# Optimization experiments

Hardware: AMD Instinct MI355X
Metric: run time of the kernel (lower is better)

Reference implementation:

```python
import jax, jax.numpy as jnp
import numpy as np

ALPHA = 0.2  # LeakyReLU negative slope
NEG_INF = -9e15

def setup_inputs() -> dict:
    key = jax.random.key(0)
    k1, k2, k3, k4 = jax.random.split(key, 4)
    N, IN_F, OUT_F = 12288, 256, 128
    h = jax.random.normal(k1, (N, IN_F), dtype=jnp.float32)
    adj = jax.random.randint(k2, (N, N), 0, 2, dtype=jnp.int32)
    # Xavier-uniform-like init with gain 1.414
    limW = 1.414 * np.sqrt(6.0 / (IN_F + OUT_F))
    W = jax.random.uniform(k3, (IN_F, OUT_F), dtype=jnp.float32, minval=-limW, maxval=limW)
    lima = 1.414 * np.sqrt(6.0 / (2 * OUT_F + 1))
    a = jax.random.uniform(k4, (2 * OUT_F, 1), dtype=jnp.float32, minval=-lima, maxval=lima)
    return {"h": h, "adj": adj, "W": W, "a": a}

def reference(h, adj, W, a):
    out_f = W.shape[1]
    Wh = h @ W                      # [N, out_f]
    Wh1 = Wh @ a[:out_f, :]         # [N, 1]
    Wh2 = Wh @ a[out_f:, :]         # [N, 1]
    e = Wh1 + Wh2.T                 # [N, N] broadcast-add scores
    e = jnp.where(e > 0, e, ALPHA * e)  # LeakyReLU
    scores = jnp.where(adj > 0, e, NEG_INF)
    attention = jax.nn.softmax(scores, axis=1)  # dropout is identity at inference
    h_prime = attention @ Wh        # [N, out_f]
    return jax.nn.elu(h_prime)      # concat=True -> ELU
```

## Files before the change

### kernel.cpp

```cpp
#include <hip/hip_runtime.h>

#define NN   12288
#define FIN  256
#define FOUT 128
#define ALPHA 0.2f

typedef __attribute__((ext_vector_type(8))) _Float16 half8v;
typedef __attribute__((ext_vector_type(4))) float float4v;
typedef __attribute__((ext_vector_type(4))) int   int4v;


#define GLL16(gp, lp)                                                          \
    __builtin_amdgcn_global_load_lds(                                          \
        (const __attribute__((address_space(1))) void*)(gp),                   \
        (__attribute__((address_space(3))) void*)(lp), 16, 0, 0)

__global__ __launch_bounds__(128) void k_wh(
    const float* __restrict__ h,
    const float* __restrict__ W,
    const float* __restrict__ a,
    _Float16* __restrict__ WhT2,
    float* __restrict__ Wh1, float* __restrict__ Wh2)
{
    __shared__ __align__(16) float hs[16 * FIN];
    __shared__ float sP1[2][16], sP2[2][16];
    const int t = threadIdx.x;
    const int row0 = blockIdx.x * 16;

    const float4v* hsrc = (const float4v*)(h + (size_t)row0 * FIN);
    float4v* hdst = (float4v*)hs;
    #pragma unroll
    for (int i = 0; i < 8; ++i) hdst[t + i * 128] = hsrc[t + i * 128];
    __syncthreads();

    float acc[16];
    #pragma unroll
    for (int r = 0; r < 16; ++r) acc[r] = 0.f;

    for (int k = 0; k < FIN; k += 4) {
        const float w0 = W[(k + 0) * FOUT + t];
        const float w1 = W[(k + 1) * FOUT + t];
        const float w2 = W[(k + 2) * FOUT + t];
        const float w3 = W[(k + 3) * FOUT + t];
        #pragma unroll
        for (int r = 0; r < 16; ++r) {
            const float4v hv = *(const float4v*)&hs[r * FIN + k];
            float s = acc[r];
            s = fmaf(hv.x, w0, s);
            s = fmaf(hv.y, w1, s);
            s = fmaf(hv.z, w2, s);
            s = fmaf(hv.w, w3, s);
            acc[r] = s;
        }
    }

    half8v pk0, pk1;
    #pragma unroll
    for (int r = 0; r < 8; ++r)  pk0[r] = (_Float16)acc[r];
    #pragma unroll
    for (int r = 0; r < 8; ++r)  pk1[r] = (_Float16)acc[8 + r];
    _Float16* dst = WhT2 + (size_t)(row0 >> 5) * 4096 + t * 32 + (row0 & 16);
    *(half8v*)(dst)     = pk0;
    *(half8v*)(dst + 8) = pk1;

    const float a1t = a[t];
    const float a2t = a[FOUT + t];
    const int lane = t & 63, wv = t >> 6;
    #pragma unroll
    for (int r = 0; r < 16; ++r) {
        float v1 = acc[r] * a1t;
        float v2 = acc[r] * a2t;
        #pragma unroll
        for (int off = 1; off < 64; off <<= 1) {
            v1 += __shfl_xor(v1, off, 64);
            v2 += __shfl_xor(v2, off, 64);
        }
        if (lane == 0) { sP1[wv][r] = v1; sP2[wv][r] = v2; }
    }
    __syncthreads();
    if (t < 16) {
        Wh1[row0 + t] = sP1[0][t] + sP1[1][t];
        Wh2[row0 + t] = sP2[0][t] + sP2[1][t];
    }
}

__global__ __launch_bounds__(256) void k_max(
    const float* __restrict__ Wh2, float* __restrict__ outmax)
{
    __shared__ float sm[4];
    float m = -1e30f;
    for (int i = threadIdx.x; i < NN; i += 256) m = fmaxf(m, Wh2[i]);
    #pragma unroll
    for (int off = 1; off < 64; off <<= 1) m = fmaxf(m, __shfl_xor(m, off, 64));
    if ((threadIdx.x & 63) == 0) sm[threadIdx.x >> 6] = m;
    __syncthreads();
    if (threadIdx.x == 0)
        outmax[0] = fmaxf(fmaxf(sm[0], sm[1]), fmaxf(sm[2], sm[3]));
}

static __device__ __forceinline__ half8v build_p(
    const int4v a0, const int4v a1, const float* wvv,
    const float wh1, const float M, float& S)
{
    const int av[8] = {a0.x, a0.y, a0.z, a0.w, a1.x, a1.y, a1.z, a1.w};
    half8v af;
    #pragma unroll
    for (int jj = 0; jj < 8; ++jj) {
        float e = wh1 + wvv[jj];
        e = fmaxf(e, ALPHA * e);
        const float p = av[jj] ? __expf(e - M) : 0.f;
        af[jj] = (_Float16)p;
        S += p;
    }
    return af;
}

__global__ __launch_bounds__(256, 3) void k_attn(
    const int* __restrict__ adj,
    const _Float16* __restrict__ WhT2,
    const float* __restrict__ Wh1, const float* __restrict__ Wh2,
    const float* __restrict__ maxp,
    float* __restrict__ pC, float* __restrict__ pS)
{
    __shared__ __align__(16) _Float16 tile[2][2][4096];
    const int tid  = threadIdx.x;
    const int w    = tid >> 6;
    const int lane = tid & 63;
    const int m    = lane & 15;
    const int q    = lane >> 4;
    const int rowbase = blockIdx.x * 128 + w * 32;
    const int J    = gridDim.y;
    const int jy   = blockIdx.y;
    const int jlen = NN / J;
    const int jbeg = jy * jlen;
    const int iters = jlen / 64;

    const float mxv  = maxp[0];
    const float wh1a = Wh1[rowbase + m];
    const float wh1b = Wh1[rowbase + 16 + m];
    const float tma = wh1a + mxv; const float Ma = fmaxf(tma, ALPHA * tma);
    const float tmb = wh1b + mxv; const float Mb = fmaxf(tmb, ALPHA * tmb);

    const int* rowA = adj + (size_t)(rowbase + m) * NN;
    const int* rowB = adj + (size_t)(rowbase + 16 + m) * NN;

    float4v c[2][8];
    #pragma unroll
    for (int rg = 0; rg < 2; ++rg)
        #pragma unroll
        for (int t = 0; t < 8; ++t) c[rg][t] = (float4v){0.f, 0.f, 0.f, 0.f};
    float Sa = 0.f, Sb = 0.f;

    {
        const float4v* grp = (const float4v*)(WhT2 + (size_t)(jbeg >> 5) * 4096);
        float4v* lb = (float4v*)&tile[0][0][0];
        #pragma unroll
        for (int k = 0; k < 4; ++k)
            GLL16(grp + (w * 4 + k) * 64 + lane, lb + (w * 4 + k) * 64);
    }
    __syncthreads();

    int buf = 0;
    for (int it = 0; it < iters; ++it) {
        const int j0 = jbeg + it * 64;

        if (it + 1 < iters) {
            const float4v* grp =
                (const float4v*)(WhT2 + (size_t)((j0 + 64) >> 5) * 4096);
            float4v* lb = (float4v*)&tile[buf ^ 1][0][0];
            #pragma unroll
            for (int k = 0; k < 4; ++k)
                GLL16(grp + (w * 4 + k) * 64 + lane, lb + (w * 4 + k) * 64);
        }

        const int jb0 = j0 + q * 8;
        const int jb1 = j0 + 32 + q * 8;
        const int4v aA0 = __builtin_nontemporal_load((const int4v*)(rowA + jb0));
        const int4v aA1 = __builtin_nontemporal_load((const int4v*)(rowA + jb0 + 4));
        const int4v aA2 = __builtin_nontemporal_load((const int4v*)(rowA + jb1));
        const int4v aA3 = __builtin_nontemporal_load((const int4v*)(rowA + jb1 + 4));
        const int4v aB0 = __builtin_nontemporal_load((const int4v*)(rowB + jb0));
        const int4v aB1 = __builtin_nontemporal_load((const int4v*)(rowB + jb0 + 4));
        const int4v aB2 = __builtin_nontemporal_load((const int4v*)(rowB + jb1));
        const int4v aB3 = __builtin_nontemporal_load((const int4v*)(rowB + jb1 + 4));
        const float4v w00 = *(const float4v*)(Wh2 + jb0);
        const float4v w01 = *(const float4v*)(Wh2 + jb0 + 4);
        const float4v w10 = *(const float4v*)(Wh2 + jb1);
        const float4v w11 = *(const float4v*)(Wh2 + jb1 + 4);
        const float wv0[8] = {w00.x, w00.y, w00.z, w00.w, w01.x, w01.y, w01.z, w01.w};
        const float wv1[8] = {w10.x, w10.y, w10.z, w10.w, w11.x, w11.y, w11.z, w11.w};

        const half8v afa0 = build_p(aA0, aA1, wv0, wh1a, Ma, Sa);
        const half8v afa1 = build_p(aA2, aA3, wv1, wh1a, Ma, Sa);
        const half8v afb0 = build_p(aB0, aB1, wv0, wh1b, Mb, Sb);
        const half8v afb1 = build_p(aB2, aB3, wv1, wh1b, Mb, Sb);

        #pragma unroll
        for (int t = 0; t < 8; ++t) {
            const half8v b = *(const half8v*)&tile[buf][0][(t * 16 + m) * 32 + q * 8];
            c[0][t] = __builtin_amdgcn_mfma_f32_16x16x32_f16(afa0, b, c[0][t], 0, 0, 0);
            c[1][t] = __builtin_amdgcn_mfma_f32_16x16x32_f16(afb0, b, c[1][t], 0, 0, 0);
        }
        #pragma unroll
        for (int t = 0; t < 8; ++t) {
            const half8v b = *(const half8v*)&tile[buf][1][(t * 16 + m) * 32 + q * 8];
            c[0][t] = __builtin_amdgcn_mfma_f32_16x16x32_f16(afa1, b, c[0][t], 0, 0, 0);
            c[1][t] = __builtin_amdgcn_mfma_f32_16x16x32_f16(afb1, b, c[1][t], 0, 0, 0);
        }

        __syncthreads();
        buf ^= 1;
    }

    Sa += __shfl_xor(Sa, 16, 64); Sa += __shfl_xor(Sa, 32, 64);
    Sb += __shfl_xor(Sb, 16, 64); Sb += __shfl_xor(Sb, 32, 64);
    if (q == 0) {
        pS[(size_t)jy * NN + rowbase + m]      = Sa;
        pS[(size_t)jy * NN + rowbase + 16 + m] = Sb;
    }
    #pragma unroll
    for (int rg = 0; rg < 2; ++rg)
        #pragma unroll
        for (int t = 0; t < 8; ++t)
            #pragma unroll
            for (int reg = 0; reg < 4; ++reg) {
                const int row = rowbase + rg * 16 + q * 4 + reg;
                pC[((size_t)jy * NN + row) * FOUT + t * 16 + m] = c[rg][t][reg];
            }
}

__global__ __launch_bounds__(256) void k_reduce(
    const float* __restrict__ pC, const float* __restrict__ pS,
    float* __restrict__ out, int J)
{
    const int idx = blockIdx.x * 256 + threadIdx.x;
    const int row = idx >> 5;
    const int c4  = (idx & 31) * 4;
    float4v acc = (float4v){0.f, 0.f, 0.f, 0.f};
    float S = 0.f;
    for (int j = 0; j < J; ++j) {
        const float4v v = *(const float4v*)(pC + ((size_t)j * NN + row) * FOUT + c4);
        acc.x += v.x; acc.y += v.y; acc.z += v.z; acc.w += v.w;
        S += pS[(size_t)j * NN + row];
    }
    const float inv = 1.f / fmaxf(S, 1e-30f);
    float4v r;
    #pragma unroll
    for (int k = 0; k < 4; ++k) {
        const float v = acc[k] * inv;
        r[k] = (v > 0.f) ? v : (__expf(v) - 1.f);
    }
    *(float4v*)(out + (size_t)row * FOUT + c4) = r;
}

__global__ __launch_bounds__(256) void k_attn_fb(
    const int* __restrict__ adj,
    const _Float16* __restrict__ WhT2,
    const float* __restrict__ Wh1, const float* __restrict__ Wh2,
    const float* __restrict__ maxp,
    float* __restrict__ out)
{
    __shared__ __align__(16) float cbuf[4][8][64][4];
    __shared__ float sbuf[4][16];
    const int tid  = threadIdx.x;
    const int w    = tid >> 6;
    const int lane = tid & 63;
    const int m    = lane & 15;
    const int q    = lane >> 4;
    const int i    = blockIdx.x * 16 + m;

    const float wh1 = Wh1[i];
    const float tm = wh1 + maxp[0];
    const float Mi = fmaxf(tm, ALPHA * tm);

    float4v c[8];
    #pragma unroll
    for (int t = 0; t < 8; ++t) c[t] = (float4v){0.f, 0.f, 0.f, 0.f};
    float S = 0.f;
    const int* adjrow = adj + (size_t)i * NN;

    for (int j0 = w * (NN / 4); j0 < (w + 1) * (NN / 4); j0 += 32) {
        const int jb = j0 + q * 8;
        const int4v  a0 = *(const int4v*)(adjrow + jb);
        const int4v  a1 = *(const int4v*)(adjrow + jb + 4);
        const float4v w0 = *(const float4v*)(Wh2 + jb);
        const float4v w1 = *(const float4v*)(Wh2 + jb + 4);
        half8v bfr[8];
        #pragma unroll
        for (int t = 0; t < 8; ++t)
            bfr[t] = *(const half8v*)(WhT2 + (size_t)(j0 >> 5) * 4096 + (t * 16 + m) * 32 + q * 8);
        const float wvv[8] = {w0.x, w0.y, w0.z, w0.w, w1.x, w1.y, w1.z, w1.w};
        const half8v af = build_p(a0, a1, wvv, wh1, Mi, S);
        #pragma unroll
        for (int t = 0; t < 8; ++t)
            c[t] = __builtin_amdgcn_mfma_f32_16x16x32_f16(af, bfr[t], c[t], 0, 0, 0);
    }
    S += __shfl_xor(S, 16, 64);
    S += __shfl_xor(S, 32, 64);
    if (lane < 16) sbuf[w][lane] = S;
    #pragma unroll
    for (int t = 0; t < 8; ++t) *(float4v*)&cbuf[w][t][lane][0] = c[t];
    __syncthreads();
    #pragma unroll
    for (int tt = 0; tt < 2; ++tt) {
        const int t = w * 2 + tt;
        float4v cs = *(const float4v*)&cbuf[0][t][lane][0];
        #pragma unroll
        for (int w2 = 1; w2 < 4; ++w2) {
            const float4v o = *(const float4v*)&cbuf[w2][t][lane][0];
            cs.x += o.x; cs.y += o.y; cs.z += o.z; cs.w += o.w;
        }
        #pragma unroll
        for (int reg = 0; reg < 4; ++reg) {
            const int mloc = q * 4 + reg;
            const float Sr = sbuf[0][mloc] + sbuf[1][mloc] + sbuf[2][mloc] + sbuf[3][mloc];
            const float v = cs[reg] / fmaxf(Sr, 1e-30f);
            out[(size_t)(blockIdx.x * 16 + mloc) * FOUT + t * 16 + m] =
                (v > 0.f) ? v : (__expf(v) - 1.f);
        }
    }
}

extern "C" void kernel_launch(void* const* d_in, const int* in_sizes, int n_in,
                              void* d_out, int out_size, void* d_ws, size_t ws_size,
                              hipStream_t stream) {
    const float* h   = (const float*)d_in[0];
    const int*   adj = (const int*)d_in[1];
    const float* W   = (const float*)d_in[2];
    const float* a   = (const float*)d_in[3];
    float* out = (float*)d_out;

    char* ws = (char*)d_ws;
    float* Wh1 = (float*)ws;
    float* Wh2 = (float*)(ws + 49152);
    float* mx  = (float*)(ws + 98304);
    _Float16* WhT2 = (_Float16*)(ws + 98560);
    const size_t base_need = 98560ULL + 3145728ULL;

    int J = 8;
    while (J > 1 &&
           base_need + (size_t)J * NN * 4 + (size_t)J * NN * FOUT * 4 > ws_size)
        J >>= 1;
    const bool ok =
        base_need + (size_t)NN * 4 + (size_t)NN * FOUT * 4 <= ws_size;

    k_wh  <<<NN / 16, 128, 0, stream>>>(h, W, a, WhT2, Wh1, Wh2);
    k_max <<<1, 256, 0, stream>>>(Wh2, mx);
    if (ok) {
        float* pS = (float*)(ws + base_need);
        float* pC = pS + (size_t)J * NN;
        k_attn<<<dim3(NN / 128, J), 256, 0, stream>>>(adj, WhT2, Wh1, Wh2, mx, pC, pS);
        k_reduce<<<(NN * (FOUT / 4)) / 256, 256, 0, stream>>>(pC, pS, out, J);
    } else {
        k_attn_fb<<<NN / 16, 256, 0, stream>>>(adj, WhT2, Wh1, Wh2, mx, out);
    }
}
```

Before: 880.9 us.

## Drop LDS staging, fuse max into projection, shrink attention tiles

The projection kernel now reads h straight from global memory instead of staging it in LDS. Each block also writes a per-block max of Wh2, so the separate max kernel is gone and every attention block reduces those partials itself. The attention kernel drops the double-buffered LDS tile of WhT2 and instead reads B fragments directly from global memory. Each wave now handles 16 rows instead of 32, so B fragments are reused across half as many rows and global/L2 traffic for WhT2 roughly doubles. The fallback kernel is reshaped the same way.

```diff
diff --git a/kernel.cpp b/kernel.cpp
--- a/kernel.cpp
+++ b/kernel.cpp
@@ -9,34 +9,24 @@
 typedef __attribute__((ext_vector_type(4))) float float4v;
 typedef __attribute__((ext_vector_type(4))) int   int4v;
 
-
-#define GLL16(gp, lp)                                                          \
-    __builtin_amdgcn_global_load_lds(                                          \
-        (const __attribute__((address_space(1))) void*)(gp),                   \
-        (__attribute__((address_space(3))) void*)(lp), 16, 0, 0)
 
 __global__ __launch_bounds__(128) void k_wh(
     const float* __restrict__ h,
     const float* __restrict__ W,
     const float* __restrict__ a,
     _Float16* __restrict__ WhT2,
-    float* __restrict__ Wh1, float* __restrict__ Wh2)
-{
-    __shared__ __align__(16) float hs[16 * FIN];
+    float* __restrict__ Wh1, float* __restrict__ Wh2,
+    float* __restrict__ mxArr)
+{
     __shared__ float sP1[2][16], sP2[2][16];
     const int t = threadIdx.x;
     const int row0 = blockIdx.x * 16;
 
-    const float4v* hsrc = (const float4v*)(h + (size_t)row0 * FIN);
-    float4v* hdst = (float4v*)hs;
-    #pragma unroll
-    for (int i = 0; i < 8; ++i) hdst[t + i * 128] = hsrc[t + i * 128];
-    __syncthreads();
-
     float acc[16];
     #pragma unroll
     for (int r = 0; r < 16; ++r) acc[r] = 0.f;
 
+    const float* hb = h + (size_t)row0 * FIN;
     for (int k = 0; k < FIN; k += 4) {
         const float w0 = W[(k + 0) * FOUT + t];
         const float w1 = W[(k + 1) * FOUT + t];
@@ -44,7 +34,7 @@
         const float w3 = W[(k + 3) * FOUT + t];
         #pragma unroll
         for (int r = 0; r < 16; ++r) {
-            const float4v hv = *(const float4v*)&hs[r * FIN + k];
+            const float4v hv = *(const float4v*)(hb + r * FIN + k);
             float s = acc[r];
             s = fmaf(hv.x, w0, s);
             s = fmaf(hv.y, w1, s);
@@ -79,23 +69,15 @@
     }
     __syncthreads();
     if (t < 16) {
-        Wh1[row0 + t] = sP1[0][t] + sP1[1][t];
-        Wh2[row0 + t] = sP2[0][t] + sP2[1][t];
-    }
-}
-
-__global__ __launch_bounds__(256) void k_max(
-    const float* __restrict__ Wh2, float* __restrict__ outmax)
-{
-    __shared__ float sm[4];
-    float m = -1e30f;
-    for (int i = threadIdx.x; i < NN; i += 256) m = fmaxf(m, Wh2[i]);
-    #pragma unroll
-    for (int off = 1; off < 64; off <<= 1) m = fmaxf(m, __shfl_xor(m, off, 64));
-    if ((threadIdx.x & 63) == 0) sm[threadIdx.x >> 6] = m;
-    __syncthreads();
-    if (threadIdx.x == 0)
-        outmax[0] = fmaxf(fmaxf(sm[0], sm[1]), fmaxf(sm[2], sm[3]));
+        const float v1 = sP1[0][t] + sP1[1][t];
+        float v2 = sP2[0][t] + sP2[1][t];
+        Wh1[row0 + t] = v1;
+        Wh2[row0 + t] = v2;
+        #pragma unroll
+        for (int off = 1; off < 16; off <<= 1)
+            v2 = fmaxf(v2, __shfl_xor(v2, off, 64));
+        if (t == 0) mxArr[blockIdx.x] = v2;
+    }
 }
 
 static __device__ __forceinline__ half8v build_p(
@@ -115,118 +97,79 @@
     return af;
 }
 
+static __device__ __forceinline__ float block_gmax(
+    const float* __restrict__ mxArr, int nmx, float* smax)
+{
+    const int tid = threadIdx.x;
+    float mv = -1e30f;
+    for (int idx = tid; idx < nmx; idx += 256) mv = fmaxf(mv, mxArr[idx]);
+    #pragma unroll
+    for (int off = 1; off < 64; off <<= 1) mv = fmaxf(mv, __shfl_xor(mv, off, 64));
+    if ((tid & 63) == 0) smax[tid >> 6] = mv;
+    __syncthreads();
+    return fmaxf(fmaxf(smax[0], smax[1]), fmaxf(smax[2], smax[3]));
+}
+
 __global__ __launch_bounds__(256, 3) void k_attn(
     const int* __restrict__ adj,
     const _Float16* __restrict__ WhT2,
     const float* __restrict__ Wh1, const float* __restrict__ Wh2,
-    const float* __restrict__ maxp,
+    const float* __restrict__ mxArr, int nmx,
     float* __restrict__ pC, float* __restrict__ pS)
 {
-    __shared__ __align__(16) _Float16 tile[2][2][4096];
+    __shared__ float smax[4];
     const int tid  = threadIdx.x;
     const int w    = tid >> 6;
     const int lane = tid & 63;
     const int m    = lane & 15;
     const int q    = lane >> 4;
-    const int rowbase = blockIdx.x * 128 + w * 32;
+    const int rowbase = blockIdx.x * 64 + w * 16;
     const int J    = gridDim.y;
     const int jy   = blockIdx.y;
     const int jlen = NN / J;
     const int jbeg = jy * jlen;
-    const int iters = jlen / 64;
-
-    const float mxv  = maxp[0];
-    const float wh1a = Wh1[rowbase + m];
-    const float wh1b = Wh1[rowbase + 16 + m];
-    const float tma = wh1a + mxv; const float Ma = fmaxf(tma, ALPHA * tma);
-    const float tmb = wh1b + mxv; const float Mb = fmaxf(tmb, ALPHA * tmb);
-
+
+    const float mxv = block_gmax(mxArr, nmx, smax);
+
+    const float wh1 = Wh1[rowbase + m];
+    const float tm  = wh1 + mxv;
+    const float Mi  = fmaxf(tm, ALPHA * tm);
     const int* rowA = adj + (size_t)(rowbase + m) * NN;
-    const int* rowB = adj + (size_t)(rowbase + 16 + m) * NN;
-
-    float4v c[2][8];
-    #pragma unroll
-    for (int rg = 0; rg < 2; ++rg)
-        #pragma unroll
-        for (int t = 0; t < 8; ++t) c[rg][t] = (float4v){0.f, 0.f, 0.f, 0.f};
-    float Sa = 0.f, Sb = 0.f;
-
-    {
-        const float4v* grp = (const float4v*)(WhT2 + (size_t)(jbeg >> 5) * 4096);
-        float4v* lb = (float4v*)&tile[0][0][0];
-        #pragma unroll
-        for (int k = 0; k < 4; ++k)
-            GLL16(grp + (w * 4 + k) * 64 + lane, lb + (w * 4 + k) * 64);
-    }
-    __syncthreads();
-
-    int buf = 0;
-    for (int it = 0; it < iters; ++it) {
-        const int j0 = jbeg + it * 64;
-
-        if (it + 1 < iters) {
-            const float4v* grp =
-                (const float4v*)(WhT2 + (size_t)((j0 + 64) >> 5) * 4096);
-            float4v* lb = (float4v*)&tile[buf ^ 1][0][0];
-            #pragma unroll
-            for (int k = 0; k < 4; ++k)
-                GLL16(grp + (w * 4 + k) * 64 + lane, lb + (w * 4 + k) * 64);
-        }
-
-        const int jb0 = j0 + q * 8;
-        const int jb1 = j0 + 32 + q * 8;
-        const int4v aA0 = __builtin_nontemporal_load((const int4v*)(rowA + jb0));
-        const int4v aA1 = __builtin_nontemporal_load((const int4v*)(rowA + jb0 + 4));
-        const int4v aA2 = __builtin_nontemporal_load((const int4v*)(rowA + jb1));
-        const int4v aA3 = __builtin_nontemporal_load((const int4v*)(rowA + jb1 + 4));
-        const int4v aB0 = __builtin_nontemporal_load((const int4v*)(rowB + jb0));
-        const int4v aB1 = __builtin_nontemporal_load((const int4v*)(rowB + jb0 + 4));
-        const int4v aB2 = __builtin_nontemporal_load((const int4v*)(rowB + jb1));
-        const int4v aB3 = __builtin_nontemporal_load((const int4v*)(rowB + jb1 + 4));
-        const float4v w00 = *(const float4v*)(Wh2 + jb0);
-        const float4v w01 = *(const float4v*)(Wh2 + jb0 + 4);
-        const float4v w10 = *(const float4v*)(Wh2 + jb1);
-        const float4v w11 = *(const float4v*)(Wh2 + jb1 + 4);
-        const float wv0[8] = {w00.x, w00.y, w00.z, w00.w, w01.x, w01.y, w01.z, w01.w};
-        const float wv1[8] = {w10.x, w10.y, w10.z, w10.w, w11.x, w11.y, w11.z, w11.w};
-
-        const half8v afa0 = build_p(aA0, aA1, wv0, wh1a, Ma, Sa);
-        const half8v afa1 = build_p(aA2, aA3, wv1, wh1a, Ma, Sa);
-        const half8v afb0 = build_p(aB0, aB1, wv0, wh1b, Mb, Sb);
-        const half8v afb1 = build_p(aB2, aB3, wv1, wh1b, Mb, Sb);
-
+
+    float4v c[8];
+    #pragma unroll
+    for (int t = 0; t < 8; ++t) c[t] = (float4v){0.f, 0.f, 0.f, 0.f};
+    float S = 0.f;
+
+    for (int j0 = jbeg; j0 < jbeg + jlen; j0 += 32) {
+        const int jb = j0 + q * 8;
+        const int4v a0 = __builtin_nontemporal_load((const int4v*)(rowA + jb));
+        const int4v a1 = __builtin_nontemporal_load((const int4v*)(rowA + jb + 4));
+        const float4v w0 = *(const float4v*)(Wh2 + jb);
+        const float4v w1 = *(const float4v*)(Wh2 + jb + 4);
+        const float wvv[8] = {w0.x, w0.y, w0.z, w0.w, w1.x, w1.y, w1.z, w1.w};
+
+        const half8v af = build_p(a0, a1, wvv, wh1, Mi, S);
+
+        const _Float16* tp = WhT2 + (size_t)(j0 >> 5) * 4096;
         #pragma unroll
         for (int t = 0; t < 8; ++t) {
-            const half8v b = *(const half8v*)&tile[buf][0][(t * 16 + m) * 32 + q * 8];
-            c[0][t] = __builtin_amdgcn_mfma_f32_16x16x32_f16(afa0, b, c[0][t], 0, 0, 0);
-            c[1][t] = __builtin_amdgcn_mfma_f32_16x16x32_f16(afb0, b, c[1][t], 0, 0, 0);
-        }
-        #pragma unroll
-        for (int t = 0; t < 8; ++t) {
-            const half8v b = *(const half8v*)&tile[buf][1][(t * 16 + m) * 32 + q * 8];
-            c[0][t] = __builtin_amdgcn_mfma_f32_16x16x32_f16(afa1, b, c[0][t], 0, 0, 0);
-            c[1][t] = __builtin_amdgcn_mfma_f32_16x16x32_f16(afb1, b, c[1][t], 0, 0, 0);
-        }
-
-        __syncthreads();
-        buf ^= 1;
-    }
-
-    Sa += __shfl_xor(Sa, 16, 64); Sa += __shfl_xor(Sa, 32, 64);
-    Sb += __shfl_xor(Sb, 16, 64); Sb += __shfl_xor(Sb, 32, 64);
-    if (q == 0) {
-        pS[(size_t)jy * NN + rowbase + m]      = Sa;
-        pS[(size_t)jy * NN + rowbase + 16 + m] = Sb;
-    }
-    #pragma unroll
-    for (int rg = 0; rg < 2; ++rg)
-        #pragma unroll
-        for (int t = 0; t < 8; ++t)
-            #pragma unroll
-            for (int reg = 0; reg < 4; ++reg) {
-                const int row = rowbase + rg * 16 + q * 4 + reg;
-                pC[((size_t)jy * NN + row) * FOUT + t * 16 + m] = c[rg][t][reg];
-            }
+            const half8v b = *(const half8v*)(tp + (t * 16 + m) * 32 + q * 8);
+            c[t] = __builtin_amdgcn_mfma_f32_16x16x32_f16(af, b, c[t], 0, 0, 0);
+        }
+    }
+
+    S += __shfl_xor(S, 16, 64);
+    S += __shfl_xor(S, 32, 64);
+    if (q == 0) pS[(size_t)jy * NN + rowbase + m] = S;
+
+    #pragma unroll
+    for (int t = 0; t < 8; ++t)
+        #pragma unroll
+        for (int reg = 0; reg < 4; ++reg) {
+            const int row = rowbase + q * 4 + reg;
+            pC[((size_t)jy * NN + row) * FOUT + t * 16 + m] = c[t][reg];
+        }
 }
 
 __global__ __launch_bounds__(256) void k_reduce(
@@ -253,69 +196,59 @@
     *(float4v*)(out + (size_t)row * FOUT + c4) = r;
 }
 
-__global__ __launch_bounds__(256) void k_attn_fb(
+__global__ __launch_bounds__(256, 3) void k_attn_fb(
     const int* __restrict__ adj,
     const _Float16* __restrict__ WhT2,
     const float* __restrict__ Wh1, const float* __restrict__ Wh2,
-    const float* __restrict__ maxp,
+    const float* __restrict__ mxArr, int nmx,
     float* __restrict__ out)
 {
-    __shared__ __align__(16) float cbuf[4][8][64][4];
-    __shared__ float sbuf[4][16];
+    __shared__ float smax[4];
     const int tid  = threadIdx.x;
     const int w    = tid >> 6;
     const int lane = tid & 63;
     const int m    = lane & 15;
     const int q    = lane >> 4;
-    const int i    = blockIdx.x * 16 + m;
-
-    const float wh1 = Wh1[i];
-    const float tm = wh1 + maxp[0];
-    const float Mi = fmaxf(tm, ALPHA * tm);
+    const int rowbase = blockIdx.x * 64 + w * 16;
+
+    const float mxv = block_gmax(mxArr, nmx, smax);
+
+    const float wh1 = Wh1[rowbase + m];
+    const float tm  = wh1 + mxv;
+    const float Mi  = fmaxf(tm, ALPHA * tm);
+    const int* rowA = adj + (size_t)(rowbase + m) * NN;
 
     float4v c[8];
     #pragma unroll
     for (int t = 0; t < 8; ++t) c[t] = (float4v){0.f, 0.f, 0.f, 0.f};
     float S = 0.f;
-    const int* adjrow = adj + (size_t)i * NN;
-
-    for (int j0 = w * (NN / 4); j0 < (w + 1) * (NN / 4); j0 += 32) {
+
+    for (int j0 = 0; j0 < NN; j0 += 32) {
         const int jb = j0 + q * 8;
-        const int4v  a0 = *(const int4v*)(adjrow + jb);
-        const int4v  a1 = *(const int4v*)(adjrow + jb + 4);
+        const int4v a0 = __builtin_nontemporal_load((const int4v*)(rowA + jb));
+        const int4v a1 = __builtin_nontemporal_load((const int4v*)(rowA + jb + 4));
         const float4v w0 = *(const float4v*)(Wh2 + jb);
         const float4v w1 = *(const float4v*)(Wh2 + jb + 4);
-        half8v bfr[8];
-        #pragma unroll
-        for (int t = 0; t < 8; ++t)
-            bfr[t] = *(const half8v*)(WhT2 + (size_t)(j0 >> 5) * 4096 + (t * 16 + m) * 32 + q * 8);
         const float wvv[8] = {w0.x, w0.y, w0.z, w0.w, w1.x, w1.y, w1.z, w1.w};
         const half8v af = build_p(a0, a1, wvv, wh1, Mi, S);
-        #pragma unroll
-        for (int t = 0; t < 8; ++t)
-            c[t] = __builtin_amdgcn_mfma_f32_16x16x32_f16(af, bfr[t], c[t], 0, 0, 0);
+        const _Float16* tp = WhT2 + (size_t)(j0 >> 5) * 4096;
+        #pragma unroll
+        for (int t = 0; t < 8; ++t) {
+            const half8v b = *(const half8v*)(tp + (t * 16 + m) * 32 + q * 8);
+            c[t] = __builtin_amdgcn_mfma_f32_16x16x32_f16(af, b, c[t], 0, 0, 0);
+        }
     }
     S += __shfl_xor(S, 16, 64);
     S += __shfl_xor(S, 32, 64);
-    if (lane < 16) sbuf[w][lane] = S;
-    #pragma unroll
-    for (int t = 0; t < 8; ++t) *(float4v*)&cbuf[w][t][lane][0] = c[t];
-    __syncthreads();
-    #pragma unroll
-    for (int tt = 0; tt < 2; ++tt) {
-        const int t = w * 2 + tt;
-        float4v cs = *(const float4v*)&cbuf[0][t][lane][0];
-        #pragma unroll
-        for (int w2 = 1; w2 < 4; ++w2) {
-            const float4v o = *(const float4v*)&cbuf[w2][t][lane][0];
-            cs.x += o.x; cs.y += o.y; cs.z += o.z; cs.w += o.w;
-        }
-        #pragma unroll
-        for (int reg = 0; reg < 4; ++reg) {
-            const int mloc = q * 4 + reg;
-            const float Sr = sbuf[0][mloc] + sbuf[1][mloc] + sbuf[2][mloc] + sbuf[3][mloc];
-            const float v = cs[reg] / fmaxf(Sr, 1e-30f);
-            out[(size_t)(blockIdx.x * 16 + mloc) * FOUT + t * 16 + m] =
+    #pragma unroll
+    for (int reg = 0; reg < 4; ++reg) {
+        const int mloc = q * 4 + reg;
+        const float Sr = __shfl(S, mloc, 64);
+        const float inv = 1.f / fmaxf(Sr, 1e-30f);
+        #pragma unroll
+        for (int t = 0; t < 8; ++t) {
+            const float v = c[t][reg] * inv;
+            out[(size_t)(rowbase + mloc) * FOUT + t * 16 + m] =
                 (v > 0.f) ? v : (__expf(v) - 1.f);
         }
     }
@@ -331,11 +264,12 @@
     float* out = (float*)d_out;
 
     char* ws = (char*)d_ws;
-    float* Wh1 = (float*)ws;
-    float* Wh2 = (float*)(ws + 49152);
-    float* mx  = (float*)(ws + 98304);
-    _Float16* WhT2 = (_Float16*)(ws + 98560);
-    const size_t base_need = 98560ULL + 3145728ULL;
+    float* Wh1   = (float*)ws;
+    float* Wh2   = (float*)(ws + 49152);
+    float* mxArr = (float*)(ws + 98304);
+    _Float16* WhT2 = (_Float16*)(ws + 101376);
+    const size_t base_need = 101376ULL + 3145728ULL;
+    const int NB = NN / 16;
 
     int J = 8;
     while (J > 1 &&
@@ -344,14 +278,14 @@
     const bool ok =
         base_need + (size_t)NN * 4 + (size_t)NN * FOUT * 4 <= ws_size;
 
-    k_wh  <<<NN / 16, 128, 0, stream>>>(h, W, a, WhT2, Wh1, Wh2);
-    k_max <<<1, 256, 0, stream>>>(Wh2, mx);
+    k_wh<<<NB, 128, 0, stream>>>(h, W, a, WhT2, Wh1, Wh2, mxArr);
     if (ok) {
         float* pS = (float*)(ws + base_need);
         float* pC = pS + (size_t)J * NN;
-        k_attn<<<dim3(NN / 128, J), 256, 0, stream>>>(adj, WhT2, Wh1, Wh2, mx, pC, pS);
+        k_attn<<<dim3(NN / 64, J), 256, 0, stream>>>(adj, WhT2, Wh1, Wh2,
+                                                     mxArr, NB, pC, pS);
         k_reduce<<<(NN * (FOUT / 4)) / 256, 256, 0, stream>>>(pC, pS, out, J);
     } else {
-        k_attn_fb<<<NN / 16, 256, 0, stream>>>(adj, WhT2, Wh1, Wh2, mx, out);
-    }
-}
+        k_attn_fb<<<NN / 64, 256, 0, stream>>>(adj, WhT2, Wh1, Wh2, mxArr, NB, out);
+    }
+}
```

Result: slower. 1.048 ms (+19.0%).
